# Kernel tuning notes

Hardware: AMD Instinct MI355X
Metric: run time of the kernel (lower is better)

Reference implementation:

```python
import jax, jax.numpy as jnp
import numpy as np

B, L, S, H, E, D = 2, 2048, 2048, 16, 64, 64

def setup_inputs() -> dict:
    key = jax.random.key(0)
    kq, kk, kv = jax.random.split(key, 3)
    queries = jax.random.normal(kq, (B, L, H, E), dtype=jnp.float32)
    keys = jax.random.normal(kk, (B, S, H, E), dtype=jnp.float32)
    values = jax.random.normal(kv, (B, S, H, D), dtype=jnp.float32)
    mask = jnp.zeros((1, 1, L, S), dtype=jnp.float32)  # additive mask, broadcast over B,H
    return {"queries": queries, "keys": keys, "values": values, "mask": mask}

def reference(queries, keys, values, mask):
    # scale defaults to 1/sqrt(E)
    scale = 1.0 / jnp.sqrt(jnp.asarray(queries.shape[-1], queries.dtype))
    # scores: [B,H,L,S]
    scores = jnp.einsum('blhe,bshe->bhls', queries, keys)
    scores = scores + mask
    A = jax.nn.softmax(scale * scores, axis=-1)  # dropout rate 0 => identity
    V = jnp.einsum('bhls,bshd->blhd', A, values)
    return V
```

## Files before the change

kernel.cpp:

```cpp
#include <hip/hip_runtime.h>

typedef _Float16 half8 __attribute__((ext_vector_type(8)));
typedef _Float16 half4 __attribute__((ext_vector_type(4)));
typedef float f32x4 __attribute__((ext_vector_type(4)));

constexpr int B = 2, L = 2048, S = 2048, H = 16, E = 64, D = 64;
constexpr int BM = 64;
constexpr int BN = 64;
constexpr int LDT = 72;

__global__ __launch_bounds__(256, 4)
void fa_kernel(const float* __restrict__ Qg, const float* __restrict__ Kg,
               const float* __restrict__ Vg, const float* __restrict__ Mg,
               float* __restrict__ Og)
{
    __shared__ _Float16 sK[BN][LDT];
    __shared__ _Float16 sV[D][LDT];

    const int tid  = threadIdx.x;
    const int wave = tid >> 6;
    const int lane = tid & 63;
    const int quad = lane >> 4;
    const int lq   = lane & 15;

    const int b  = blockIdx.y >> 4;
    const int h  = blockIdx.y & 15;
    const int q0 = blockIdx.x * BM;

    const int rowStride = H * E;
    const size_t qbase = ((size_t)b * L) * rowStride + h * E;
    const size_t kbase = ((size_t)b * S) * rowStride + h * E;

    const float cS = 0.125f * 1.44269504089f;

    half8 qf[2];
    {
        const float* qp = Qg + qbase + (size_t)(q0 + wave*16 + lq) * rowStride + quad*8;
        #pragma unroll
        for (int ks = 0; ks < 2; ++ks)
            #pragma unroll
            for (int j = 0; j < 8; ++j)
                qf[ks][j] = (_Float16)(qp[ks*32 + j] * cS);
    }

    const float* mrow = Mg + (size_t)(q0 + wave*16 + lq) * S;

    float lsum = 0.f;
    f32x4 oacc[4];
    #pragma unroll
    for (int dt = 0; dt < 4; ++dt) oacc[dt] = (f32x4){0.f, 0.f, 0.f, 0.f};

    const int db = tid & 15;
    const int sb = tid >> 4;

    for (int s0 = 0; s0 < S; s0 += BN) {
        #pragma unroll
        for (int i = 0; i < 4; ++i) {
            int idx = i * 256 + tid;
            int r  = idx >> 4;
            int c  = (idx & 15) * 4;
            const float4 kv = *(const float4*)(Kg + kbase + (size_t)(s0 + r) * rowStride + c);
            half4 hk = {(_Float16)kv.x, (_Float16)kv.y, (_Float16)kv.z, (_Float16)kv.w};
            *(half4*)&sK[r][c] = hk;
        }
        {
            const float* vp = Vg + kbase + (size_t)(s0 + sb*4) * rowStride + db*4;
            float4 vr[4];
            #pragma unroll
            for (int i = 0; i < 4; ++i)
                vr[i] = *(const float4*)(vp + (size_t)i * rowStride);
            const int sOff = (((sb >> 1) ^ (db & 7)) << 3) + ((sb & 1) << 2);
            #pragma unroll
            for (int j = 0; j < 4; ++j) {
                half4 hv = { (_Float16)((&vr[0].x)[j]), (_Float16)((&vr[1].x)[j]),
                             (_Float16)((&vr[2].x)[j]), (_Float16)((&vr[3].x)[j]) };
                *(half4*)&sV[db*4 + j][sOff] = hv;
            }
        }
        __syncthreads();

        float4 mv[4];
        #pragma unroll
        for (int nt = 0; nt < 4; ++nt)
            mv[nt] = *(const float4*)(mrow + s0 + nt*16 + quad*4);

        f32x4 sf[4];
        #pragma unroll
        for (int nt = 0; nt < 4; ++nt) {
            half8 kf0 = *(const half8*)&sK[nt*16 + lq][ 0 + quad*8];
            half8 kf1 = *(const half8*)&sK[nt*16 + lq][32 + quad*8];
            f32x4 acc = (f32x4){0.f, 0.f, 0.f, 0.f};
            acc = __builtin_amdgcn_mfma_f32_16x16x32_f16(kf0, qf[0], acc, 0, 0, 0);
            acc = __builtin_amdgcn_mfma_f32_16x16x32_f16(kf1, qf[1], acc, 0, 0, 0);
            sf[nt] = acc;
        }

        half4 pf[4];
        #pragma unroll
        for (int nt = 0; nt < 4; ++nt) {
            #pragma unroll
            for (int r = 0; r < 4; ++r) {
                float lg = fmaf((&mv[nt].x)[r], cS, sf[nt][r]);
                float p  = __builtin_amdgcn_exp2f(lg);
                lsum += p;
                pf[nt][r] = (_Float16)p;
            }
        }

        #pragma unroll
        for (int nt = 0; nt < 4; ++nt) {
            const int s8 = nt*2 + (quad >> 1);
            const int wOff = (quad & 1) << 2;
            #pragma unroll
            for (int dt = 0; dt < 4; ++dt) {
                const int vrow = dt*16 + lq;
                const int phys = ((s8 ^ ((vrow >> 2) & 7)) << 3) + wOff;
                half4 vf = *(const half4*)&sV[vrow][phys];
                oacc[dt] = __builtin_amdgcn_mfma_f32_16x16x16f16(pf[nt], vf, oacc[dt], 0, 0, 0);
            }
        }
        __syncthreads();
    }

    lsum += __shfl_xor(lsum, 16);
    lsum += __shfl_xor(lsum, 32);

    #pragma unroll
    for (int r = 0; r < 4; ++r) {
        float l_bc = __shfl(lsum, quad*4 + r, 16);
        float inv = 1.f / l_bc;
        float* orow = Og + qbase + (size_t)(q0 + wave*16 + quad*4 + r) * rowStride;
        #pragma unroll
        for (int dt = 0; dt < 4; ++dt)
            orow[dt*16 + lq] = oacc[dt][r] * inv;
    }
}

extern "C" void kernel_launch(void* const* d_in, const int* in_sizes, int n_in,
                              void* d_out, int out_size, void* d_ws, size_t ws_size,
                              hipStream_t stream) {
    const float* Qg = (const float*)d_in[0];
    const float* Kg = (const float*)d_in[1];
    const float* Vg = (const float*)d_in[2];
    const float* Mg = (const float*)d_in[3];
    float* Og = (float*)d_out;
    dim3 grid(L / BM, B * H);
    fa_kernel<<<grid, 256, 0, stream>>>(Qg, Kg, Vg, Mg, Og);
}
```

Measured before the change: 209.7 us.

## Prefetch next K/V/mask tiles into registers and use 16x16x32 MFMA for PV

Global loads of the next K, V and mask tiles are issued into registers while the current tile is computed, so memory latency overlaps with the MFMA and exp work. Probabilities are staged through a per-wave LDS buffer so the PV product can use the wider 16x16x32 f16 MFMA with half8 operands. The V swizzle is changed to match the new 8-wide reads. This costs extra registers and LDS plus an LDS round-trip for P, which may reduce occupancy under launch_bounds(256,4).

```diff
diff --git a/kernel.cpp b/kernel.cpp
--- a/kernel.cpp
+++ b/kernel.cpp
@@ -8,6 +8,7 @@
 constexpr int BM = 64;
 constexpr int BN = 64;
 constexpr int LDT = 72;
+constexpr int NTI = S / BN;
 
 __global__ __launch_bounds__(256, 4)
 void fa_kernel(const float* __restrict__ Qg, const float* __restrict__ Kg,
@@ -16,6 +17,7 @@
 {
     __shared__ _Float16 sK[BN][LDT];
     __shared__ _Float16 sV[D][LDT];
+    __shared__ _Float16 sP[4][16][LDT];
 
     const int tid  = threadIdx.x;
     const int wave = tid >> 6;
@@ -52,37 +54,46 @@
 
     const int db = tid & 15;
     const int sb = tid >> 4;
+    const float* vbase = Vg + kbase + (size_t)(sb*4) * rowStride + db*4;
 
-    for (int s0 = 0; s0 < S; s0 += BN) {
+    float4 kreg[4], vreg[4], mreg[4];
+    #pragma unroll
+    for (int i = 0; i < 4; ++i) {
+        int idx = i*256 + tid;
+        kreg[i] = *(const float4*)(Kg + kbase + (size_t)(idx >> 4) * rowStride + (idx & 15)*4);
+        vreg[i] = *(const float4*)(vbase + (size_t)i * rowStride);
+        mreg[i] = *(const float4*)(mrow + i*16 + quad*4);
+    }
+
+    for (int t = 0; t < NTI; ++t) {
         #pragma unroll
         for (int i = 0; i < 4; ++i) {
-            int idx = i * 256 + tid;
-            int r  = idx >> 4;
-            int c  = (idx & 15) * 4;
-            const float4 kv = *(const float4*)(Kg + kbase + (size_t)(s0 + r) * rowStride + c);
-            half4 hk = {(_Float16)kv.x, (_Float16)kv.y, (_Float16)kv.z, (_Float16)kv.w};
+            int idx = i*256 + tid;
+            int r = idx >> 4, c = (idx & 15)*4;
+            half4 hk = {(_Float16)kreg[i].x, (_Float16)kreg[i].y,
+                        (_Float16)kreg[i].z, (_Float16)kreg[i].w};
             *(half4*)&sK[r][c] = hk;
         }
         {
-            const float* vp = Vg + kbase + (size_t)(s0 + sb*4) * rowStride + db*4;
-            float4 vr[4];
-            #pragma unroll
-            for (int i = 0; i < 4; ++i)
-                vr[i] = *(const float4*)(vp + (size_t)i * rowStride);
-            const int sOff = (((sb >> 1) ^ (db & 7)) << 3) + ((sb & 1) << 2);
+            const int off = (((sb >> 1) ^ (db >> 1)) << 3) + ((sb & 1) << 2);
             #pragma unroll
             for (int j = 0; j < 4; ++j) {
-                half4 hv = { (_Float16)((&vr[0].x)[j]), (_Float16)((&vr[1].x)[j]),
-                             (_Float16)((&vr[2].x)[j]), (_Float16)((&vr[3].x)[j]) };
-                *(half4*)&sV[db*4 + j][sOff] = hv;
+                half4 hv = { (_Float16)((&vreg[0].x)[j]), (_Float16)((&vreg[1].x)[j]),
+                             (_Float16)((&vreg[2].x)[j]), (_Float16)((&vreg[3].x)[j]) };
+                *(half4*)&sV[db*4 + j][off] = hv;
             }
         }
         __syncthreads();
 
-        float4 mv[4];
-        #pragma unroll
-        for (int nt = 0; nt < 4; ++nt)
-            mv[nt] = *(const float4*)(mrow + s0 + nt*16 + quad*4);
+        if (t + 1 < NTI) {
+            const int s0n = (t + 1) * BN;
+            #pragma unroll
+            for (int i = 0; i < 4; ++i) {
+                int idx = i*256 + tid;
+                kreg[i] = *(const float4*)(Kg + kbase + (size_t)(s0n + (idx >> 4)) * rowStride + (idx & 15)*4);
+                vreg[i] = *(const float4*)(vbase + (size_t)(s0n + i) * rowStride);
+            }
+        }
 
         f32x4 sf[4];
         #pragma unroll
@@ -95,28 +106,35 @@
             sf[nt] = acc;
         }
 
-        half4 pf[4];
         #pragma unroll
         for (int nt = 0; nt < 4; ++nt) {
+            half4 hp;
             #pragma unroll
             for (int r = 0; r < 4; ++r) {
-                float lg = fmaf((&mv[nt].x)[r], cS, sf[nt][r]);
+                float lg = fmaf((&mreg[nt].x)[r], cS, sf[nt][r]);
                 float p  = __builtin_amdgcn_exp2f(lg);
                 lsum += p;
-                pf[nt][r] = (_Float16)p;
+                hp[r] = (_Float16)p;
             }
+            *(half4*)&sP[wave][lq][nt*16 + quad*4] = hp;
+        }
+
+        if (t + 1 < NTI) {
+            const int s0n = (t + 1) * BN;
+            #pragma unroll
+            for (int nt = 0; nt < 4; ++nt)
+                mreg[nt] = *(const float4*)(mrow + s0n + nt*16 + quad*4);
         }
 
         #pragma unroll
-        for (int nt = 0; nt < 4; ++nt) {
-            const int s8 = nt*2 + (quad >> 1);
-            const int wOff = (quad & 1) << 2;
+        for (int ks = 0; ks < 2; ++ks) {
+            half8 pf = *(const half8*)&sP[wave][lq][ks*32 + quad*8];
             #pragma unroll
             for (int dt = 0; dt < 4; ++dt) {
                 const int vrow = dt*16 + lq;
-                const int phys = ((s8 ^ ((vrow >> 2) & 7)) << 3) + wOff;
-                half4 vf = *(const half4*)&sV[vrow][phys];
-                oacc[dt] = __builtin_amdgcn_mfma_f32_16x16x16f16(pf[nt], vf, oacc[dt], 0, 0, 0);
+                const int phys = (ks*4 + quad) ^ ((vrow >> 3) & 7);
+                half8 vf = *(const half8*)&sV[vrow][phys << 3];
+                oacc[dt] = __builtin_amdgcn_mfma_f32_16x16x32_f16(pf, vf, oacc[dt], 0, 0, 0);
             }
         }
         __syncthreads();
```

New measurement: 218.2 us. +4.0%, slower.

## Stage P through LDS to use 16x16x32 MFMA for PV and remap grid

Applied to the files above, without the earlier changes.

Each wave now writes its probability tile to a per-wave LDS buffer and reads it back as half8 fragments, so the PV product can use the wider 16x16x32 f16 MFMA with half8 V reads under a new swizzle. This halves the number of PV MFMA instructions and widens the V loads from LDS. The cost is extra LDS writes and reads for P plus more shared memory per block, which may lower occupancy. The grid is also flattened to 1D with a remap that spreads batch-head pairs across consecutive blocks, aiming for better cache locality or load spreading.

```diff
diff --git a/kernel.cpp b/kernel.cpp
--- a/kernel.cpp
+++ b/kernel.cpp
@@ -8,6 +8,7 @@
 constexpr int BM = 64;
 constexpr int BN = 64;
 constexpr int LDT = 72;
+constexpr int NTI = S / BN;
 
 __global__ __launch_bounds__(256, 4)
 void fa_kernel(const float* __restrict__ Qg, const float* __restrict__ Kg,
@@ -16,6 +17,7 @@
 {
     __shared__ _Float16 sK[BN][LDT];
     __shared__ _Float16 sV[D][LDT];
+    __shared__ _Float16 sP[4][16][LDT];
 
     const int tid  = threadIdx.x;
     const int wave = tid >> 6;
@@ -23,9 +25,12 @@
     const int quad = lane >> 4;
     const int lq   = lane & 15;
 
-    const int b  = blockIdx.y >> 4;
-    const int h  = blockIdx.y & 15;
-    const int q0 = blockIdx.x * BM;
+    const int i  = blockIdx.x;
+    const int bh = (i & 7) * 4 + ((i >> 3) & 3);
+    const int qb = i >> 5;
+    const int b  = bh >> 4;
+    const int h  = bh & 15;
+    const int q0 = qb * BM;
 
     const int rowStride = H * E;
     const size_t qbase = ((size_t)b * L) * rowStride + h * E;
@@ -52,29 +57,29 @@
 
     const int db = tid & 15;
     const int sb = tid >> 4;
+    const float* vbase = Vg + kbase + (size_t)(sb*4) * rowStride + db*4;
 
-    for (int s0 = 0; s0 < S; s0 += BN) {
+    for (int t = 0; t < NTI; ++t) {
+        const int s0 = t * BN;
         #pragma unroll
-        for (int i = 0; i < 4; ++i) {
-            int idx = i * 256 + tid;
-            int r  = idx >> 4;
-            int c  = (idx & 15) * 4;
+        for (int ii = 0; ii < 4; ++ii) {
+            int idx = ii*256 + tid;
+            int r = idx >> 4, c = (idx & 15)*4;
             const float4 kv = *(const float4*)(Kg + kbase + (size_t)(s0 + r) * rowStride + c);
             half4 hk = {(_Float16)kv.x, (_Float16)kv.y, (_Float16)kv.z, (_Float16)kv.w};
             *(half4*)&sK[r][c] = hk;
         }
         {
-            const float* vp = Vg + kbase + (size_t)(s0 + sb*4) * rowStride + db*4;
             float4 vr[4];
             #pragma unroll
-            for (int i = 0; i < 4; ++i)
-                vr[i] = *(const float4*)(vp + (size_t)i * rowStride);
-            const int sOff = (((sb >> 1) ^ (db & 7)) << 3) + ((sb & 1) << 2);
+            for (int j = 0; j < 4; ++j)
+                vr[j] = *(const float4*)(vbase + (size_t)(s0 + j) * rowStride);
+            const int off = (((sb >> 1) ^ (db >> 1)) << 3) + ((sb & 1) << 2);
             #pragma unroll
             for (int j = 0; j < 4; ++j) {
                 half4 hv = { (_Float16)((&vr[0].x)[j]), (_Float16)((&vr[1].x)[j]),
                              (_Float16)((&vr[2].x)[j]), (_Float16)((&vr[3].x)[j]) };
-                *(half4*)&sV[db*4 + j][sOff] = hv;
+                *(half4*)&sV[db*4 + j][off] = hv;
             }
         }
         __syncthreads();
@@ -95,28 +100,28 @@
             sf[nt] = acc;
         }
 
-        half4 pf[4];
         #pragma unroll
         for (int nt = 0; nt < 4; ++nt) {
+            half4 hp;
             #pragma unroll
             for (int r = 0; r < 4; ++r) {
                 float lg = fmaf((&mv[nt].x)[r], cS, sf[nt][r]);
                 float p  = __builtin_amdgcn_exp2f(lg);
                 lsum += p;
-                pf[nt][r] = (_Float16)p;
+                hp[r] = (_Float16)p;
             }
+            *(half4*)&sP[wave][lq][nt*16 + quad*4] = hp;
         }
 
         #pragma unroll
-        for (int nt = 0; nt < 4; ++nt) {
-            const int s8 = nt*2 + (quad >> 1);
-            const int wOff = (quad & 1) << 2;
+        for (int ks = 0; ks < 2; ++ks) {
+            half8 pf = *(const half8*)&sP[wave][lq][ks*32 + quad*8];
             #pragma unroll
             for (int dt = 0; dt < 4; ++dt) {
                 const int vrow = dt*16 + lq;
-                const int phys = ((s8 ^ ((vrow >> 2) & 7)) << 3) + wOff;
-                half4 vf = *(const half4*)&sV[vrow][phys];
-                oacc[dt] = __builtin_amdgcn_mfma_f32_16x16x16f16(pf[nt], vf, oacc[dt], 0, 0, 0);
+                const int phys = (ks*4 + quad) ^ ((vrow >> 3) & 7);
+                half8 vf = *(const half8*)&sV[vrow][phys << 3];
+                oacc[dt] = __builtin_amdgcn_mfma_f32_16x16x32_f16(pf, vf, oacc[dt], 0, 0, 0);
             }
         }
         __syncthreads();
@@ -144,6 +149,6 @@
     const float* Vg = (const float*)d_in[2];
     const float* Mg = (const float*)d_in[3];
     float* Og = (float*)d_out;
-    dim3 grid(L / BM, B * H);
+    dim3 grid((L / BM) * B * H);
     fa_kernel<<<grid, 256, 0, stream>>>(Qg, Kg, Vg, Mg, Og);
 }
```

New measurement: 195.9 us. 6.6% less time.
